# Kernel optimization log

Measured on AMD Instinct MI355X. Metric: run time of the kernel, lower is better.

## Reference

```python
import jax, jax.numpy as jnp
import numpy as np

G = 16                 # grid side -> 4096 voxels
N_GRID = G ** 3
N_NODES = 4096         # protein nodes
DEG = 256              # node neighbors per grid voxel
HID = 64               # MPNN hidden == ResNet in_channels
NUM_CLASSES = 20
BN = np.float32(1.0 / np.sqrt(1.0 + 1e-5))  # eval-mode BatchNorm3d (mean=0, var=1, gamma=1, beta=0)


def _lin(key, fi, fo):
    return jax.random.normal(key, (fi, fo), jnp.float32) * (fi ** -0.5)


def _cw(key, o, i, k):
    return jax.random.normal(key, (o, i, k, k, k), jnp.float32) * ((i * k ** 3) ** -0.5)


def setup_inputs() -> dict:
    key = jax.random.key(0)
    ks = jax.random.split(key, 32)
    n_edges = N_GRID * DEG
    # every grid voxel receives exactly DEG messages (bincount never zero)
    edge_i = jax.random.randint(ks[0], (n_edges,), 0, N_NODES, dtype=jnp.int32)
    edge_j = jnp.repeat(jnp.arange(N_GRID, dtype=jnp.int32), DEG)
    edge_index = jnp.stack([edge_i, edge_j])  # [2, E]

    node_embedding = jax.random.normal(ks[1], (N_NODES, HID), jnp.float32)
    node_pos = jax.random.uniform(ks[2], (N_NODES, 3), jnp.float32)
    gx = (jnp.arange(G, dtype=jnp.float32) + 0.5) / G
    gd, gh, gw = jnp.meshgrid(gx, gx, gx, indexing='ij')
    grid_pos = jnp.stack([gd, gh, gw], -1).reshape(N_GRID, 3)

    z = lambda n: jnp.zeros((n,), jnp.float32)
    return {
        'node_embedding': node_embedding, 'node_pos': node_pos,
        'grid_pos': grid_pos, 'edge_index': edge_index,
        # MPNN edge / message / update MLPs
        'ew1': _lin(ks[3], 6, HID), 'eb1': z(HID), 'ew2': _lin(ks[4], HID, HID), 'eb2': z(HID),
        'mw1': _lin(ks[5], 2 * HID, HID), 'mb1': z(HID), 'mw2': _lin(ks[6], HID, HID), 'mb2': z(HID),
        'uw1': _lin(ks[7], HID, HID), 'ub1': z(HID), 'uw2': _lin(ks[8], HID, HID), 'ub2': z(HID),
        # ResNet3D: 3 Blocks (conv3 a, conv3 b, conv5 shortcut) with channels 64->64, 64->128, 128->256
        'c1a': _cw(ks[9], 64, 64, 3), 'c1b': _cw(ks[10], 64, 64, 3), 'c1s': _cw(ks[11], 64, 64, 5),
        'c2a': _cw(ks[12], 128, 64, 3), 'c2b': _cw(ks[13], 128, 128, 3), 'c2s': _cw(ks[14], 128, 64, 5),
        'c3a': _cw(ks[15], 256, 128, 3), 'c3b': _cw(ks[16], 256, 256, 3), 'c3s': _cw(ks[17], 256, 128, 5),
        'fcw': _lin(ks[18], 256, NUM_CLASSES), 'fcb': z(NUM_CLASSES),
    }


def _mlp(x, w1, b1, w2, b2):
    return jax.nn.silu(x @ w1 + b1) @ w2 + b2


def _conv(x, w, p):
    return jax.lax.conv_general_dilated(
        x, w, window_strides=(1, 1, 1), padding=[(p, p)] * 3,
        dimension_numbers=('NCDHW', 'OIDHW', 'NCDHW'))


def _block(x, wa, wb, ws):
    out = jax.nn.relu(_conv(x, wa, 1) * BN)
    out = _conv(out, wb, 1) * BN
    sc = _conv(x, ws, 2) * BN
    return jax.nn.relu(out + sc)


def reference(node_embedding, node_pos, grid_pos, edge_index,
              ew1, eb1, ew2, eb2, mw1, mb1, mw2, mb2, uw1, ub1, uw2, ub2,
              c1a, c1b, c1s, c2a, c2b, c2s, c3a, c3b, c3s, fcw, fcb):
    i, j = edge_index[0], edge_index[1]
    # ---- MPNN: gather, edge MLP, message MLP, scatter-mean, update MLP ----
    edge_attr = jnp.concatenate([node_pos[i], grid_pos[j]], axis=-1)        # [E, 6]
    pos_emb = _mlp(edge_attr, ew1, eb1, ew2, eb2)                           # [E, H]
    msg = _mlp(jnp.concatenate([node_embedding[i], pos_emb], -1),
               mw1, mb1, mw2, mb2)                                          # [E, H]
    agg = jax.ops.segment_sum(msg, j, num_segments=N_GRID)                  # [N_GRID, H]
    cnt = jax.ops.segment_sum(jnp.ones((msg.shape[0],), msg.dtype), j,
                              num_segments=N_GRID)
    grid_feat = _mlp(agg / cnt[:, None], uw1, ub1, uw2, ub2)                # [N_GRID, H]
    # ---- ResNet3D over the grid volume ----
    x = grid_feat.T.reshape(1, HID, G, G, G) * BN                           # instance_norm1 (eval BN)
    x = _block(x, c1a, c1b, c1s)
    x = _block(x, c2a, c2b, c2s)
    x = _block(x, c3a, c3b, c3s)
    pooled = jnp.max(x, axis=(2, 3, 4))                                     # max_pool3d(kernel=spatial)
    return pooled @ fcw + fcb                                               # [1, NUM_CLASSES]
```

## Files before the change

kernel.cpp:

```cpp
#include <hip/hip_runtime.h>
#include <math.h>

#define BN_S 0.9999950000374997f

typedef _Float16 half8 __attribute__((ext_vector_type(8)));
typedef float f32x4 __attribute__((ext_vector_type(4)));

__device__ __forceinline__ float silu_f(float x) {
    return __fdividef(x, 1.0f + __expf(-x));
}

__device__ __forceinline__ void gld16(const void* g, void* l) {
    __builtin_amdgcn_global_load_lds(
        (const __attribute__((address_space(1))) void*)g,
        (__attribute__((address_space(3))) void*)l, 16, 0, 0);
}

__global__ __launch_bounds__(64) void prep_w_k(
    const float* __restrict__ ew2, const float* __restrict__ mw1,
    const float* __restrict__ mw2, const float* __restrict__ uw1,
    const float* __restrict__ mb2, const float* __restrict__ ub1,
    float* __restrict__ W_mu, float* __restrict__ b_mu,
    _Float16* __restrict__ wemt_h, _Float16* __restrict__ wemt_l)
{
    const int k = blockIdx.x, c = threadIdx.x;
    float s = 0.f;
    for (int m = 0; m < 64; m++) s = fmaf(ew2[k*64 + m], mw1[(64 + m)*64 + c], s);
    {
        const int q = k >> 5, kg = (k >> 3) & 3, jj = k & 7;
        const int sl = q*256 + c*4 + kg;
        const int p = sl ^ ((sl >> 3) & 7);
        const _Float16 h = (_Float16)s;
        const _Float16 l = (_Float16)(s - (float)h);
        wemt_h[p*8 + jj] = h;
        wemt_l[p*8 + jj] = l;
    }
    float s2 = 0.f;
    for (int m = 0; m < 64; m++) s2 = fmaf(mw2[k*64 + m], uw1[m*64 + c], s2);
    W_mu[k*64 + c] = s2;
    if (k == 0) {
        float s3 = ub1[c];
        for (int m = 0; m < 64; m++) s3 = fmaf(mb2[m], uw1[m*64 + c], s3);
        b_mu[c] = s3;
    }
}

__global__ __launch_bounds__(64) void prep_nodes_k(
    const float* __restrict__ node_embedding, const float* __restrict__ node_pos,
    const float* __restrict__ grid_pos, const float* __restrict__ ew1,
    const float* __restrict__ eb1, const float* __restrict__ mw1,
    const float* __restrict__ mb1, const float* __restrict__ eb2,
    float* __restrict__ a_node, float* __restrict__ g_vox, float* __restrict__ n_node)
{
    const int v = blockIdx.x, c = threadIdx.x;
    const float p0 = node_pos[v*3], p1 = node_pos[v*3 + 1], p2 = node_pos[v*3 + 2];
    a_node[v*64 + c] = fmaf(p0, ew1[c], fmaf(p1, ew1[64 + c], fmaf(p2, ew1[128 + c], eb1[c])));
    const float q0 = grid_pos[v*3], q1 = grid_pos[v*3 + 1], q2 = grid_pos[v*3 + 2];
    g_vox[v*64 + c] = fmaf(q0, ew1[192 + c], fmaf(q1, ew1[256 + c], q2 * ew1[320 + c]));
    float s = mb1[c];
    for (int k = 0; k < 64; k++) s = fmaf(node_embedding[v*64 + k], mw1[k*64 + c], s);
    for (int k = 0; k < 64; k++) s = fmaf(eb2[k], mw1[(64 + k)*64 + c], s);
    n_node[v*64 + c] = s;
}

template<int K3, int NCOG, int NCH>
__global__ __launch_bounds__(256) void wsplit_k(
    const float* __restrict__ w, _Float16* __restrict__ dh, _Float16* __restrict__ dl,
    int CI)
{
    __shared__ float s[32*K3];
    const int co = blockIdx.x, cig = blockIdx.y, t = threadIdx.x;
    const float* src = w + ((size_t)co*CI + cig*32)*K3;
    for (int m = t; m < 32*K3; m += 256) s[m] = src[m];
    __syncthreads();
    const int coG = co >> 6, col = co & 63;
    for (int m = t; m < 32*K3; m += 256) {
        const int tap = m >> 5, cil = m & 31;
        const float x = s[cil*K3 + tap];
        const _Float16 h = (_Float16)x;
        const _Float16 l = (_Float16)(x - (float)h);
        const int b = cil >> 3, jj = cil & 7;
        const int sl = col*4 + b;
        const int p = sl ^ ((sl >> 3) & 7);
        const size_t base = ((size_t)(tap*NCOG + coG)*NCH + cig) * 2048;
        dh[base + p*8 + jj] = h;
        dl[base + p*8 + jj] = l;
    }
}

__global__ __launch_bounds__(256) void edge_kernel(
    const int* __restrict__ edge_i,
    const float* __restrict__ a_node, const float* __restrict__ g_vox,
    const float* __restrict__ n_node,
    const _Float16* __restrict__ wemt_h, const _Float16* __restrict__ wemt_l,
    const float* __restrict__ W_mu, const float* __restrict__ b_mu,
    const float* __restrict__ uw2, const float* __restrict__ ub2,
    _Float16* __restrict__ x0h, _Float16* __restrict__ x0l)
{
    __shared__ __align__(16) _Float16 sAh[4096], sAl[4096];
    __shared__ __align__(16) _Float16 sBh[4096], sBl[4096];
    __shared__ float sV1[64], sV2[64];

    const int j = blockIdx.x, t = threadIdx.x;
    const int lane = t & 63, wv = t >> 6, ln15 = lane & 15, kg = lane >> 4;
    const int ebase = j << 8;

    gld16(wemt_h + t*8, &sAh[t*8]);
    gld16(wemt_h + 2048 + t*8, &sAh[2048 + t*8]);
    gld16(wemt_l + t*8, &sAl[t*8]);
    gld16(wemt_l + 2048 + t*8, &sAl[2048 + t*8]);

    const int r = t >> 2, sub = t & 3;
    float gv[16];
    #pragma unroll
    for (int m = 0; m < 16; m++) gv[m] = g_vox[j*64 + sub*16 + m];

    asm volatile("s_waitcnt vmcnt(0)" ::: "memory");
    __syncthreads();

    float psum[4] = {0.f, 0.f, 0.f, 0.f};

    for (int T = 0; T < 4; T++) {
        {
            const int i = edge_i[ebase + T*64 + r];
            float s1[16];
            #pragma unroll
            for (int m = 0; m < 16; m++)
                s1[m] = silu_f(a_node[i*64 + sub*16 + m] + gv[m]);
            half8 h0, l0, h1, l1;
            #pragma unroll
            for (int m = 0; m < 8; m++) {
                h0[m] = (_Float16)s1[m];
                l0[m] = (_Float16)(s1[m] - (float)h0[m]);
                h1[m] = (_Float16)s1[8 + m];
                l1[m] = (_Float16)(s1[8 + m] - (float)h1[m]);
            }
            const int q = sub >> 1, kg0 = (sub & 1) * 2;
            const int slot0 = (q*4 + kg0)*64 + r;
            *(half8*)&sBh[slot0*8] = h0; *(half8*)&sBl[slot0*8] = l0;
            *(half8*)&sBh[(slot0 + 64)*8] = h1; *(half8*)&sBl[(slot0 + 64)*8] = l1;
        }
        __syncthreads();
        #pragma unroll
        for (int eF = 0; eF < 4; eF++) {
            const int e = eF*16 + ln15;
            const int ie = edge_i[ebase + T*64 + e];
            f32x4 acc;
            {
                const float4 nv = *(const float4*)&n_node[(size_t)ie*64 + wv*16 + kg*4];
                acc[0] = nv.x; acc[1] = nv.y; acc[2] = nv.z; acc[3] = nv.w;
            }
            #pragma unroll
            for (int q = 0; q < 2; q++) {
                const int sa = q*256 + (wv*16 + ln15)*4 + kg;
                const int pa = sa ^ ((sa >> 3) & 7);
                const half8 Ah = *(const half8*)&sAh[pa*8];
                const half8 Al = *(const half8*)&sAl[pa*8];
                const int sb = ((q*4 + kg)*64 + e)*8;
                const half8 Bh = *(const half8*)&sBh[sb];
                const half8 Bl = *(const half8*)&sBl[sb];
                acc = __builtin_amdgcn_mfma_f32_16x16x32_f16(Ah, Bh, acc, 0, 0, 0);
                acc = __builtin_amdgcn_mfma_f32_16x16x32_f16(Ah, Bl, acc, 0, 0, 0);
                acc = __builtin_amdgcn_mfma_f32_16x16x32_f16(Al, Bh, acc, 0, 0, 0);
            }
            #pragma unroll
            for (int rg = 0; rg < 4; rg++) psum[rg] += silu_f(acc[rg]);
        }
        __syncthreads();
    }

    #pragma unroll
    for (int rg = 0; rg < 4; rg++) {
        float v = psum[rg];
        v += __shfl_xor(v, 1, 64); v += __shfl_xor(v, 2, 64);
        v += __shfl_xor(v, 4, 64); v += __shfl_xor(v, 8, 64);
        psum[rg] = v;
    }
    if (ln15 == 0) {
        #pragma unroll
        for (int rg = 0; rg < 4; rg++)
            sV1[wv*16 + kg*4 + rg] = psum[rg] * (1.0f / 256.0f);
    }
    __syncthreads();
    if (t < 64) {
        float h = b_mu[t];
        for (int k = 0; k < 64; k++) h = fmaf(sV1[k], W_mu[k*64 + t], h);
        sV2[t] = silu_f(h);
    }
    __syncthreads();
    if (t < 64) {
        float g = ub2[t];
        for (int k = 0; k < 64; k++) g = fmaf(sV2[k], uw2[k*64 + t], g);
        const float val = g * BN_S;
        const _Float16 hh = (_Float16)val;
        const _Float16 ll = (_Float16)(val - (float)hh);
        const int c = t, zz = j >> 8, v = j & 255;
        const int oct = (c >> 3) & 3;
        const int vsw = v ^ (oct << 1);
        const size_t a16 = ((size_t)((c >> 5)*16 + zz)*1024 + oct*256 + vsw)*8 + (c & 7);
        x0h[a16] = hh; x0l[a16] = ll;
    }
}

template<int KK, int CI, int NCO32, int CIS>
__global__ __launch_bounds__(256, 4) void conv_mfma_k(
    const _Float16* __restrict__ xh, const _Float16* __restrict__ xl,
    const _Float16* __restrict__ wh, const _Float16* __restrict__ wl,
    float* __restrict__ slab)
{
    constexpr int P = KK/2, K2 = KK*KK, NCH = CI/32, NCHS = NCH/CIS;
    constexpr int CO = NCO32*32, NCOG64 = NCO32/2;
    const int d0 = blockIdx.x, coG32 = blockIdx.y;
    const int co64G = coG32 >> 1, coHalf = coG32 & 1;
    const int cis = blockIdx.z / KK, kd = blockIdx.z % KK;
    const int t = threadIdx.x;
    const int lane = t & 63, wv = t >> 6;
    const int ln15 = lane & 15, kg = lane >> 4;

    float* sout = slab + ((size_t)blockIdx.z*CO + coG32*32)*4096 + d0*256;
    const int z = d0 + kd - P;
    if ((unsigned)z >= 16u) {
        for (int m = t; m < 32*256; m += 256)
            sout[(size_t)(m >> 8)*4096 + (m & 255)] = 0.f;
        return;
    }

    __shared__ __align__(16) _Float16 sXh[8192];
    __shared__ __align__(16) _Float16 sXl[8192];
    __shared__ __align__(16) _Float16 zb[8];
    if (t < 8) zb[t] = (_Float16)0.f;

    int aoff[2];
    #pragma unroll
    for (int cf = 0; cf < 2; cf++) {
        const int s = (coHalf*32 + cf*16 + ln15)*4 + kg;
        aoff[cf] = (s ^ ((s >> 3) & 7)) * 8;
    }

    auto stage_X = [&](int ch) {
        const size_t b16 = ((size_t)ch*16 + z) * 8192;
        #pragma unroll
        for (int q = 0; q < 4; q++) {
            gld16(xh + b16 + (q*256 + t)*8, &sXh[(q*256 + t)*8]);
            gld16(xl + b16 + (q*256 + t)*8, &sXl[(q*256 + t)*8]);
        }
    };
    auto loadA = [&](int ch, int t2, half8* Ah, half8* Al) {
        const size_t b = ((size_t)((kd*K2 + t2)*NCOG64 + co64G)*NCH + ch) * 2048;
        #pragma unroll
        for (int cf = 0; cf < 2; cf++) {
            Ah[cf] = *(const half8*)&wh[b + aoff[cf]];
            Al[cf] = *(const half8*)&wl[b + aoff[cf]];
        }
    };

    f32x4 acc[2][4];
    #pragma unroll
    for (int a = 0; a < 2; a++)
        #pragma unroll
        for (int b = 0; b < 4; b++)
            #pragma unroll
            for (int r2 = 0; r2 < 4; r2++) acc[a][b][r2] = 0.f;

    const int ch0 = cis * NCHS;
    half8 nAh[2], nAl[2];
    stage_X(ch0);
    loadA(ch0, 0, nAh, nAl);
    asm volatile("s_waitcnt vmcnt(0)" ::: "memory");
    __syncthreads();

    for (int cc = 0; cc < NCHS; cc++) {
        const int ch = ch0 + cc;
        for (int t2 = 0; t2 < K2; t2++) {
            half8 cAh[2], cAl[2];
            #pragma unroll
            for (int cf = 0; cf < 2; cf++) { cAh[cf] = nAh[cf]; cAl[cf] = nAl[cf]; }
            if (t2 + 1 < K2)          loadA(ch, t2 + 1, nAh, nAl);
            else if (cc + 1 < NCHS)   loadA(ch + 1, 0, nAh, nAl);

            const int kh = t2 / KK, kw = t2 % KK;
            __builtin_amdgcn_s_setprio(1);
            #pragma unroll
            for (int f = 0; f < 4; f++) {
                const int h_in = wv*4 + f + kh - P;
                if ((unsigned)h_in < 16u) {
                    const int w_in = ln15 + kw - P;
                    const bool ok = (unsigned)w_in < 16u;
                    const int slot = ok ? (kg*256 + h_in*16 + (w_in ^ (kg << 1))) : 0;
                    const half8 Bh = ok ? *(const half8*)&sXh[slot*8] : *(const half8*)zb;
                    const half8 Bl = ok ? *(const half8*)&sXl[slot*8] : *(const half8*)zb;
                    #pragma unroll
                    for (int cf = 0; cf < 2; cf++) {
                        acc[cf][f] = __builtin_amdgcn_mfma_f32_16x16x32_f16(cAh[cf], Bh, acc[cf][f], 0, 0, 0);
                        acc[cf][f] = __builtin_amdgcn_mfma_f32_16x16x32_f16(cAh[cf], Bl, acc[cf][f], 0, 0, 0);
                        acc[cf][f] = __builtin_amdgcn_mfma_f32_16x16x32_f16(cAl[cf], Bh, acc[cf][f], 0, 0, 0);
                    }
                }
            }
            __builtin_amdgcn_s_setprio(0);
        }
        if (cc + 1 < NCHS) {
            __syncthreads();
            stage_X(ch + 1);
            asm volatile("s_waitcnt vmcnt(0)" ::: "memory");
            __syncthreads();
        }
    }

    #pragma unroll
    for (int cf = 0; cf < 2; cf++)
        #pragma unroll
        for (int f = 0; f < 4; f++)
            #pragma unroll
            for (int r2 = 0; r2 < 4; r2++)
                sout[(size_t)(cf*16 + kg*4 + r2)*4096 + wv*64 + f*16 + ln15] = acc[cf][f][r2];
}

template<int S, int RMODE, int OUT>
__global__ __launch_bounds__(256) void reduce_k(
    const float* __restrict__ pbuf, const float* __restrict__ addsrc,
    float* __restrict__ outf, _Float16* __restrict__ oh, _Float16* __restrict__ ol,
    int CO)
{
    const int z = blockIdx.x, c8 = blockIdx.y, v = threadIdx.x;
    float val[8];
    #pragma unroll
    for (int jj = 0; jj < 8; jj++) {
        const int c = c8*8 + jj;
        float a = 0.f;
        #pragma unroll
        for (int s = 0; s < S; s++)
            a += pbuf[((size_t)s*CO + c)*4096 + z*256 + v];
        a *= BN_S;
        if (RMODE == 3) a += addsrc[(size_t)c*4096 + z*256 + v];
        if (RMODE != 2) a = fmaxf(a, 0.f);
        val[jj] = a;
    }
    if (OUT == 0) {
        #pragma unroll
        for (int jj = 0; jj < 8; jj++)
            outf[(size_t)(c8*8 + jj)*4096 + z*256 + v] = val[jj];
    } else if (OUT == 1) {
        half8 hv, lv;
        #pragma unroll
        for (int jj = 0; jj < 8; jj++) {
            hv[jj] = (_Float16)val[jj];
            lv[jj] = (_Float16)(val[jj] - (float)hv[jj]);
        }
        const int oct = c8 & 3;
        const int vsw = v ^ (oct << 1);
        const size_t a16 = ((size_t)((c8 >> 2)*16 + z)*1024 + oct*256 + vsw)*8;
        *(half8*)&oh[a16] = hv;
        *(half8*)&ol[a16] = lv;
    } else {
        __shared__ float sm[4][8];
        #pragma unroll
        for (int jj = 0; jj < 8; jj++) {
            float m = val[jj];
            m = fmaxf(m, __shfl_xor(m, 1, 64));  m = fmaxf(m, __shfl_xor(m, 2, 64));
            m = fmaxf(m, __shfl_xor(m, 4, 64));  m = fmaxf(m, __shfl_xor(m, 8, 64));
            m = fmaxf(m, __shfl_xor(m, 16, 64)); m = fmaxf(m, __shfl_xor(m, 32, 64));
            if ((v & 63) == 0) sm[v >> 6][jj] = m;
        }
        __syncthreads();
        if (v < 8) {
            const float m = fmaxf(fmaxf(sm[0][v], sm[1][v]), fmaxf(sm[2][v], sm[3][v]));
            outf[z*CO + c8*8 + v] = m;
        }
    }
}

__global__ __launch_bounds__(256) void fc_k(
    const float* __restrict__ pp, const float* __restrict__ fcw,
    const float* __restrict__ fcb, float* __restrict__ out)
{
    __shared__ float sp[256];
    const int t = threadIdx.x;
    float m = pp[t];
    for (int zz = 1; zz < 16; zz++) m = fmaxf(m, pp[zz*256 + t]);
    sp[t] = m;
    __syncthreads();
    if (t < 20) {
        float s = fcb[t];
        for (int c = 0; c < 256; c++) s = fmaf(sp[c], fcw[c*20 + t], s);
        out[t] = s;
    }
}

extern "C" void kernel_launch(void* const* d_in, const int* in_sizes, int n_in,
                              void* d_out, int out_size, void* d_ws, size_t ws_size,
                              hipStream_t stream)
{
    const float* node_embedding = (const float*)d_in[0];
    const float* node_pos       = (const float*)d_in[1];
    const float* grid_pos       = (const float*)d_in[2];
    const int*   edge_index     = (const int*)d_in[3];
    const float* ew1 = (const float*)d_in[4];
    const float* eb1 = (const float*)d_in[5];
    const float* ew2 = (const float*)d_in[6];
    const float* eb2 = (const float*)d_in[7];
    const float* mw1 = (const float*)d_in[8];
    const float* mb1 = (const float*)d_in[9];
    const float* mw2 = (const float*)d_in[10];
    const float* mb2 = (const float*)d_in[11];
    const float* uw1 = (const float*)d_in[12];
    const float* ub1 = (const float*)d_in[13];
    const float* uw2 = (const float*)d_in[14];
    const float* ub2 = (const float*)d_in[15];
    const float* c1a = (const float*)d_in[16];
    const float* c1b = (const float*)d_in[17];
    const float* c1s = (const float*)d_in[18];
    const float* c2a = (const float*)d_in[19];
    const float* c2b = (const float*)d_in[20];
    const float* c2s = (const float*)d_in[21];
    const float* c3a = (const float*)d_in[22];
    const float* c3b = (const float*)d_in[23];
    const float* c3s = (const float*)d_in[24];
    const float* fcw = (const float*)d_in[25];
    const float* fcb = (const float*)d_in[26];
    float* out = (float*)d_out;
    const int* edge_i = edge_index;

    float* ws = (float*)d_ws;
    float* a_node = ws;                ws += 262144;
    float* g_vox  = ws;                ws += 262144;
    float* n_node = ws;                ws += 262144;
    float* W_mu   = ws;                ws += 4096;
    float* b_mu   = ws;                ws += 64;
    _Float16* wemt_h = (_Float16*)ws;  ws += 2048;
    _Float16* wemt_l = (_Float16*)ws;  ws += 2048;
    _Float16* x0h = (_Float16*)ws;     ws += 131072;
    _Float16* x0l = (_Float16*)ws;     ws += 131072;
    _Float16* t2h = (_Float16*)ws;     ws += 262144;
    _Float16* t2l = (_Float16*)ws;     ws += 262144;
    _Float16* x2h = (_Float16*)ws;     ws += 262144;
    _Float16* x2l = (_Float16*)ws;     ws += 262144;
    _Float16* t3h = (_Float16*)ws;     ws += 524288;
    _Float16* t3l = (_Float16*)ws;     ws += 524288;
    float* u2 = ws;                    ws += 524288;
    float* u3 = ws;                    ws += 1048576;
    float* slab = ws;                  ws += 5242880;
    float* poolPart = ws;              ws += 4096;
    _Float16* wh = (_Float16*)ws;      ws += 4585472;
    _Float16* wl = (_Float16*)ws;      ws += 4585472;
    _Float16* t1h = (_Float16*)a_node;
    _Float16* t1l = (_Float16*)(a_node + 131072);
    float* u1 = g_vox;
    _Float16* x1h = (_Float16*)n_node;
    _Float16* x1l = (_Float16*)(n_node + 131072);

    _Float16* w1a_h = wh + 0;       _Float16* w1a_l = wl + 0;
    _Float16* w1b_h = wh + 110592;  _Float16* w1b_l = wl + 110592;
    _Float16* w1s_h = wh + 221184;  _Float16* w1s_l = wl + 221184;
    _Float16* w2a_h = wh + 733184;  _Float16* w2a_l = wl + 733184;
    _Float16* w2b_h = wh + 954368;  _Float16* w2b_l = wl + 954368;
    _Float16* w2s_h = wh + 1396736; _Float16* w2s_l = wl + 1396736;
    _Float16* w3a_h = wh + 2420736; _Float16* w3a_l = wl + 2420736;
    _Float16* w3b_h = wh + 3305472; _Float16* w3b_l = wl + 3305472;
    _Float16* w3s_h = wh + 5074944; _Float16* w3s_l = wl + 5074944;

    hipLaunchKernelGGL((wsplit_k<27,1,2>),  dim3(64,2),  dim3(256), 0, stream, c1a, w1a_h, w1a_l, 64);
    hipLaunchKernelGGL((wsplit_k<27,1,2>),  dim3(64,2),  dim3(256), 0, stream, c1b, w1b_h, w1b_l, 64);
    hipLaunchKernelGGL((wsplit_k<125,1,2>), dim3(64,2),  dim3(256), 0, stream, c1s, w1s_h, w1s_l, 64);
    hipLaunchKernelGGL((wsplit_k<27,2,2>),  dim3(128,2), dim3(256), 0, stream, c2a, w2a_h, w2a_l, 64);
    hipLaunchKernelGGL((wsplit_k<27,2,4>),  dim3(128,4), dim3(256), 0, stream, c2b, w2b_h, w2b_l, 128);
    hipLaunchKernelGGL((wsplit_k<125,2,2>), dim3(128,2), dim3(256), 0, stream, c2s, w2s_h, w2s_l, 64);
    hipLaunchKernelGGL((wsplit_k<27,4,4>),  dim3(256,4), dim3(256), 0, stream, c3a, w3a_h, w3a_l, 128);
    hipLaunchKernelGGL((wsplit_k<27,4,8>),  dim3(256,8), dim3(256), 0, stream, c3b, w3b_h, w3b_l, 256);
    hipLaunchKernelGGL((wsplit_k<125,4,4>), dim3(256,4), dim3(256), 0, stream, c3s, w3s_h, w3s_l, 128);

    hipLaunchKernelGGL(prep_w_k, dim3(64), dim3(64), 0, stream,
                       ew2, mw1, mw2, uw1, mb2, ub1, W_mu, b_mu, wemt_h, wemt_l);
    hipLaunchKernelGGL(prep_nodes_k, dim3(4096), dim3(64), 0, stream,
                       node_embedding, node_pos, grid_pos, ew1, eb1, mw1, mb1, eb2,
                       a_node, g_vox, n_node);
    hipLaunchKernelGGL(edge_kernel, dim3(4096), dim3(256), 0, stream,
                       edge_i, a_node, g_vox, n_node, wemt_h, wemt_l,
                       W_mu, b_mu, uw2, ub2, x0h, x0l);

    hipLaunchKernelGGL((conv_mfma_k<3,64,2,2>), dim3(16,2,6), dim3(256), 0, stream, x0h, x0l, w1a_h, w1a_l, slab);
    hipLaunchKernelGGL((reduce_k<6,1,1>), dim3(16,8), dim3(256), 0, stream, slab, (const float*)nullptr, (float*)nullptr, t1h, t1l, 64);
    hipLaunchKernelGGL((conv_mfma_k<3,64,2,2>), dim3(16,2,6), dim3(256), 0, stream, t1h, t1l, w1b_h, w1b_l, slab);
    hipLaunchKernelGGL((reduce_k<6,2,0>), dim3(16,8), dim3(256), 0, stream, slab, (const float*)nullptr, u1, (_Float16*)nullptr, (_Float16*)nullptr, 64);
    hipLaunchKernelGGL((conv_mfma_k<5,64,2,2>), dim3(16,2,10), dim3(256), 0, stream, x0h, x0l, w1s_h, w1s_l, slab);
    hipLaunchKernelGGL((reduce_k<10,3,1>), dim3(16,8), dim3(256), 0, stream, slab, u1, (float*)nullptr, x1h, x1l, 64);
    hipLaunchKernelGGL((conv_mfma_k<3,64,4,2>), dim3(16,4,6), dim3(256), 0, stream, x1h, x1l, w2a_h, w2a_l, slab);
    hipLaunchKernelGGL((reduce_k<6,1,1>), dim3(16,16), dim3(256), 0, stream, slab, (const float*)nullptr, (float*)nullptr, t2h, t2l, 128);
    hipLaunchKernelGGL((conv_mfma_k<3,128,4,2>), dim3(16,4,6), dim3(256), 0, stream, t2h, t2l, w2b_h, w2b_l, slab);
    hipLaunchKernelGGL((reduce_k<6,2,0>), dim3(16,16), dim3(256), 0, stream, slab, (const float*)nullptr, u2, (_Float16*)nullptr, (_Float16*)nullptr, 128);
    hipLaunchKernelGGL((conv_mfma_k<5,64,4,2>), dim3(16,4,10), dim3(256), 0, stream, x1h, x1l, w2s_h, w2s_l, slab);
    hipLaunchKernelGGL((reduce_k<10,3,1>), dim3(16,16), dim3(256), 0, stream, slab, u2, (float*)nullptr, x2h, x2l, 128);
    hipLaunchKernelGGL((conv_mfma_k<3,128,8,1>), dim3(16,8,3), dim3(256), 0, stream, x2h, x2l, w3a_h, w3a_l, slab);
    hipLaunchKernelGGL((reduce_k<3,1,1>), dim3(16,32), dim3(256), 0, stream, slab, (const float*)nullptr, (float*)nullptr, t3h, t3l, 256);
    hipLaunchKernelGGL((conv_mfma_k<3,256,8,1>), dim3(16,8,3), dim3(256), 0, stream, t3h, t3l, w3b_h, w3b_l, slab);
    hipLaunchKernelGGL((reduce_k<3,2,0>), dim3(16,32), dim3(256), 0, stream, slab, (const float*)nullptr, u3, (_Float16*)nullptr, (_Float16*)nullptr, 256);
    hipLaunchKernelGGL((conv_mfma_k<5,128,8,1>), dim3(16,8,5), dim3(256), 0, stream, x2h, x2l, w3s_h, w3s_l, slab);
    hipLaunchKernelGGL((reduce_k<5,3,2>), dim3(16,32), dim3(256), 0, stream, slab, u3, poolPart, (_Float16*)nullptr, (_Float16*)nullptr, 256);

    hipLaunchKernelGGL(fc_k, dim3(1), dim3(256), 0, stream, poolPart, fcw, fcb, out);

    (void)in_sizes; (void)n_in; (void)out_size; (void)ws_size;
}
```

Baseline: 538.4 us.

## Double-buffer edge gathers in registers and split per-voxel MLP across all waves

The edge kernel now prefetches the next tile's a_node rows and n_node slices into registers while the current tile is converted and multiplied, so the gather latency overlaps the MFMA work. The loads are vectorized as float4. The two 64x64 per-voxel matvecs after the edge loop are split across all four waves, with a shared-memory reduction, instead of running on a single wave. This costs more registers, which the launch bound of 3 blocks is meant to contain, plus a few extra barriers.

```diff
diff --git a/kernel.cpp b/kernel.cpp
--- a/kernel.cpp
+++ b/kernel.cpp
@@ -88,7 +88,7 @@
     }
 }
 
-__global__ __launch_bounds__(256) void edge_kernel(
+__global__ __launch_bounds__(256, 3) void edge_kernel(
     const int* __restrict__ edge_i,
     const float* __restrict__ a_node, const float* __restrict__ g_vox,
     const float* __restrict__ n_node,
@@ -99,7 +99,7 @@
 {
     __shared__ __align__(16) _Float16 sAh[4096], sAl[4096];
     __shared__ __align__(16) _Float16 sBh[4096], sBl[4096];
-    __shared__ float sV1[64], sV2[64];
+    __shared__ float sV1[64], sV2[64], sRed[4*64];
 
     const int j = blockIdx.x, t = threadIdx.x;
     const int lane = t & 63, wv = t >> 6, ln15 = lane & 15, kg = lane >> 4;
@@ -111,22 +111,42 @@
     gld16(wemt_l + 2048 + t*8, &sAl[2048 + t*8]);
 
     const int r = t >> 2, sub = t & 3;
-    float gv[16];
-    #pragma unroll
-    for (int m = 0; m < 16; m++) gv[m] = g_vox[j*64 + sub*16 + m];
+    float4 gv4[4];
+    #pragma unroll
+    for (int m4 = 0; m4 < 4; m4++)
+        gv4[m4] = *(const float4*)&g_vox[j*64 + sub*16 + m4*4];
+
+    float4 A[2][4], N[2][4];
+    {
+        const int iA = edge_i[ebase + r];
+        #pragma unroll
+        for (int m4 = 0; m4 < 4; m4++)
+            A[0][m4] = *(const float4*)&a_node[(size_t)iA*64 + sub*16 + m4*4];
+        #pragma unroll
+        for (int eF = 0; eF < 4; eF++) {
+            const int ieX = edge_i[ebase + eF*16 + ln15];
+            N[0][eF] = *(const float4*)&n_node[(size_t)ieX*64 + wv*16 + kg*4];
+        }
+    }
 
     asm volatile("s_waitcnt vmcnt(0)" ::: "memory");
     __syncthreads();
 
     float psum[4] = {0.f, 0.f, 0.f, 0.f};
 
+    #pragma unroll
     for (int T = 0; T < 4; T++) {
+        const int par = T & 1;
         {
-            const int i = edge_i[ebase + T*64 + r];
             float s1[16];
             #pragma unroll
-            for (int m = 0; m < 16; m++)
-                s1[m] = silu_f(a_node[i*64 + sub*16 + m] + gv[m]);
+            for (int m4 = 0; m4 < 4; m4++) {
+                const float4 a = A[par][m4], g = gv4[m4];
+                s1[m4*4 + 0] = silu_f(a.x + g.x);
+                s1[m4*4 + 1] = silu_f(a.y + g.y);
+                s1[m4*4 + 2] = silu_f(a.z + g.z);
+                s1[m4*4 + 3] = silu_f(a.w + g.w);
+            }
             half8 h0, l0, h1, l1;
             #pragma unroll
             for (int m = 0; m < 8; m++) {
@@ -140,14 +160,25 @@
             *(half8*)&sBh[slot0*8] = h0; *(half8*)&sBl[slot0*8] = l0;
             *(half8*)&sBh[(slot0 + 64)*8] = h1; *(half8*)&sBl[(slot0 + 64)*8] = l1;
         }
+        if (T < 3) {
+            const int b1 = ebase + (T + 1)*64;
+            const int iA = edge_i[b1 + r];
+            #pragma unroll
+            for (int m4 = 0; m4 < 4; m4++)
+                A[par ^ 1][m4] = *(const float4*)&a_node[(size_t)iA*64 + sub*16 + m4*4];
+            #pragma unroll
+            for (int eF = 0; eF < 4; eF++) {
+                const int ieX = edge_i[b1 + eF*16 + ln15];
+                N[par ^ 1][eF] = *(const float4*)&n_node[(size_t)ieX*64 + wv*16 + kg*4];
+            }
+        }
         __syncthreads();
         #pragma unroll
         for (int eF = 0; eF < 4; eF++) {
             const int e = eF*16 + ln15;
-            const int ie = edge_i[ebase + T*64 + e];
             f32x4 acc;
             {
-                const float4 nv = *(const float4*)&n_node[(size_t)ie*64 + wv*16 + kg*4];
+                const float4 nv = N[par][eF];
                 acc[0] = nv.x; acc[1] = nv.y; acc[2] = nv.z; acc[3] = nv.w;
             }
             #pragma unroll
@@ -182,16 +213,33 @@
             sV1[wv*16 + kg*4 + rg] = psum[rg] * (1.0f / 256.0f);
     }
     __syncthreads();
+    {
+        const int c = t & 63, part = t >> 6;
+        float h = (part == 0) ? b_mu[c] : 0.f;
+        #pragma unroll
+        for (int k2 = 0; k2 < 16; k2++) {
+            const int k = part*16 + k2;
+            h = fmaf(sV1[k], W_mu[k*64 + c], h);
+        }
+        sRed[part*64 + c] = h;
+    }
+    __syncthreads();
+    if (t < 64)
+        sV2[t] = silu_f(sRed[t] + sRed[64 + t] + sRed[128 + t] + sRed[192 + t]);
+    __syncthreads();
+    {
+        const int c = t & 63, part = t >> 6;
+        float g = (part == 0) ? ub2[c] : 0.f;
+        #pragma unroll
+        for (int k2 = 0; k2 < 16; k2++) {
+            const int k = part*16 + k2;
+            g = fmaf(sV2[k], uw2[k*64 + c], g);
+        }
+        sRed[part*64 + c] = g;
+    }
+    __syncthreads();
     if (t < 64) {
-        float h = b_mu[t];
-        for (int k = 0; k < 64; k++) h = fmaf(sV1[k], W_mu[k*64 + t], h);
-        sV2[t] = silu_f(h);
-    }
-    __syncthreads();
-    if (t < 64) {
-        float g = ub2[t];
-        for (int k = 0; k < 64; k++) g = fmaf(sV2[k], uw2[k*64 + t], g);
-        const float val = g * BN_S;
+        const float val = (sRed[t] + sRed[64 + t] + sRed[128 + t] + sRed[192 + t]) * BN_S;
         const _Float16 hh = (_Float16)val;
         const _Float16 ll = (_Float16)(val - (float)hh);
         const int c = t, zz = j >> 8, v = j & 255;
```

After: 540.5 us. About the same (+0.4%).
